# Kernel optimization log

Hardware: AMD Instinct MI355X
Metric: run time of the kernel (lower is better)

The kernel has to match this reference:

```python
import jax, jax.numpy as jnp
import numpy as np


def _square_distance(src, dst):
    # src: [B,N,C], dst: [B,M,C] -> [B,N,M] squared euclidean distances
    # ||s-d||^2 = -2 s.d + ||s||^2 + ||d||^2
    d = -2.0 * jnp.einsum('bnc,bmc->bnm', src, dst)
    d = d + jnp.sum(src * src, axis=-1)[:, :, None]
    d = d + jnp.sum(dst * dst, axis=-1)[:, None, :]
    return d


def setup_inputs() -> dict:
    key = jax.random.key(0)
    k1, k2 = jax.random.split(key)
    B, N, M, C = 8, 4096, 4096, 3
    f = jax.random.normal(k1, (B, N, C), dtype=jnp.float32)
    f_ = jax.random.normal(k2, (B, M, C), dtype=jnp.float32)
    return {"f": f, "f_": f_}


def reference(f, f_):
    dis = _square_distance(f, f_)          # [B,N,M]
    f2f_ = jnp.min(dis, axis=2)            # [B,N] nearest in f_ for each f point
    f_2f = jnp.min(dis, axis=1)            # [B,M] nearest in f for each f_ point
    d = jnp.mean(f2f_, axis=1) + jnp.mean(f_2f, axis=1)  # [B]
    return jnp.mean(d)
```

## Files before the change

### kernel.cpp

```cpp
#include <hip/hip_runtime.h>


typedef __attribute__((ext_vector_type(8))) short bf16x8;
typedef __attribute__((ext_vector_type(4))) float f32x4;

constexpr int B = 8;
constexpr int N = 4096;
constexpr int M = 4096;

constexpr int ROWS_PER_BLOCK = 128;
constexpr int COLS_PER_BLOCK = 2048;
constexpr int SEG = 512;
constexpr int SEGS = COLS_PER_BLOCK / SEG;
constexpr int TILES = SEG / 16;

static __device__ __forceinline__ unsigned short f2bf(float v) {
    unsigned u = __float_as_uint(v);
    return (unsigned short)((u + 0x7FFFu + ((u >> 16) & 1u)) >> 16);
}
static __device__ __forceinline__ float bf2f(unsigned short b) {
    return __uint_as_float(((unsigned)b) << 16);
}
static __device__ __forceinline__ void split3(float v, unsigned short& a,
                                              unsigned short& b, unsigned short& c) {
    a = f2bf(v); float r = v - bf2f(a);
    b = f2bf(r); r -= bf2f(b);
    c = f2bf(r);
}

__global__ __launch_bounds__(256, 4) void chamfer_dir_mfma(
    const float* __restrict__ f,
    const float* __restrict__ f_,
    unsigned int* __restrict__ minA,
    unsigned int* __restrict__ minB)
{
    __shared__ bf16x8 Bt[TILES * 64];

    const int tid  = threadIdx.x;
    const int lane = tid & 63;
    const int w    = tid >> 6;
    const int r    = lane & 15;
    const int kg   = lane >> 4;

    const int dir = blockIdx.z;
    const int b   = blockIdx.y;
    const int rc  = blockIdx.x >> 1;
    const int ch  = blockIdx.x & 1;

    const float* qsrc = dir ? f_ : f;
    const float* tsrc = dir ? f  : f_;
    unsigned int* omin = dir ? minB : minA;

    const int rowbase = rc * ROWS_PER_BLOCK + w * 32;
    bf16x8 afrag[2];
    #pragma unroll
    for (int rt = 0; rt < 2; ++rt) {
        const float* qp = qsrc + ((size_t)b * N + rowbase + rt * 16 + r) * 3;
        const float x = qp[0], y = qp[1], z = qp[2];
        unsigned short px0,px1,px2, py0,py1,py2, pz0,pz1,pz2, n0,n1,n2;
        split3(-2.f * x, px0, px1, px2);
        split3(-2.f * y, py0, py1, py2);
        split3(-2.f * z, pz0, pz1, pz2);
        split3(x*x + y*y + z*z, n0, n1, n2);
        const short ONE = 0x3F80;
        bf16x8 a;
        if (kg == 0)
            a = (bf16x8){(short)px0,(short)px0,(short)px1,(short)px1,(short)px0,(short)px2,(short)py0,(short)py0};
        else if (kg == 1)
            a = (bf16x8){(short)py1,(short)py1,(short)py0,(short)py2,(short)pz0,(short)pz0,(short)pz1,(short)pz1};
        else if (kg == 2)
            a = (bf16x8){(short)pz0,(short)pz2,(short)n0,(short)n1,(short)n2,ONE,ONE,ONE};
        else
            a = (bf16x8){0,0,0,0,0,0,0,0};
        afrag[rt] = a;
    }

    float rm[2][4];
    #pragma unroll
    for (int j = 0; j < 4; ++j) { rm[0][j] = 3.402823466e+38f; rm[1][j] = 3.402823466e+38f; }

    const float* tb = tsrc + ((size_t)b * M + (size_t)ch * COLS_PER_BLOCK) * 3;
    const f32x4 zero = {0.f, 0.f, 0.f, 0.f};

    for (int s = 0; s < SEGS; ++s) {
        __syncthreads();
        #pragma unroll
        for (int i = 0; i < 2; ++i) {
            const int t = i * 256 + tid;
            const float* tp = tb + (size_t)(s * SEG + t) * 3;
            const float x = tp[0], y = tp[1], z = tp[2];
            unsigned short x0,x1,x2, y0,y1,y2, z0,z1,z2, m0,m1,m2;
            split3(x, x0, x1, x2);
            split3(y, y0, y1, y2);
            split3(z, z0, z1, z2);
            split3(x*x + y*y + z*z, m0, m1, m2);
            const short ONE = 0x3F80;
            const int tile = t >> 4, rr = t & 15;
            bf16x8* base = &Bt[tile * 64 + rr];
            base[ 0] = (bf16x8){(short)x0,(short)x1,(short)x0,(short)x1,(short)x2,(short)x0,(short)y0,(short)y1};
            base[16] = (bf16x8){(short)y0,(short)y1,(short)y2,(short)y0,(short)z0,(short)z1,(short)z0,(short)z1};
            base[32] = (bf16x8){(short)z2,(short)z0,ONE,ONE,ONE,(short)m0,(short)m1,(short)m2};
            base[48] = (bf16x8){0,0,0,0,0,0,0,0};
        }
        __syncthreads();

        bf16x8 bb = Bt[lane];
        f32x4 pc0 = __builtin_amdgcn_mfma_f32_16x16x32_bf16(afrag[0], bb, zero, 0, 0, 0);
        f32x4 pc1 = __builtin_amdgcn_mfma_f32_16x16x32_bf16(afrag[1], bb, zero, 0, 0, 0);
        #pragma unroll 4
        for (int ct = 1; ct < TILES; ++ct) {
            bb = Bt[ct * 64 + lane];
            f32x4 c0 = __builtin_amdgcn_mfma_f32_16x16x32_bf16(afrag[0], bb, zero, 0, 0, 0);
            f32x4 c1 = __builtin_amdgcn_mfma_f32_16x16x32_bf16(afrag[1], bb, zero, 0, 0, 0);
            #pragma unroll
            for (int j = 0; j < 4; ++j) {
                rm[0][j] = fminf(rm[0][j], pc0[j]);
                rm[1][j] = fminf(rm[1][j], pc1[j]);
            }
            pc0 = c0; pc1 = c1;
        }
        #pragma unroll
        for (int j = 0; j < 4; ++j) {
            rm[0][j] = fminf(rm[0][j], pc0[j]);
            rm[1][j] = fminf(rm[1][j], pc1[j]);
        }
    }

    #pragma unroll
    for (int rt = 0; rt < 2; ++rt) {
        #pragma unroll
        for (int j = 0; j < 4; ++j) {
            float v = rm[rt][j];
            v = fminf(v, __shfl_xor(v, 1));
            v = fminf(v, __shfl_xor(v, 2));
            v = fminf(v, __shfl_xor(v, 4));
            v = fminf(v, __shfl_xor(v, 8));
            if (r == 0) {
                const int row = rowbase + rt * 16 + kg * 4 + j;
                atomicMin(&omin[b * N + row], __float_as_uint(v));
            }
        }
    }
}

__global__ __launch_bounds__(256) void reduce_out_kernel(
    const uint4* __restrict__ mins,
    float* __restrict__ out)
{
    __shared__ float wsum[4];
    const int tid = threadIdx.x;
    const uint4 v = mins[blockIdx.x * 256 + tid];
    float s = (__uint_as_float(v.x) + __uint_as_float(v.y))
            + (__uint_as_float(v.z) + __uint_as_float(v.w));

    #pragma unroll
    for (int off = 32; off > 0; off >>= 1) s += __shfl_down(s, off, 64);
    if ((tid & 63) == 0) wsum[tid >> 6] = s;
    __syncthreads();
    if (tid == 0) {
        const float r = (wsum[0] + wsum[1]) + (wsum[2] + wsum[3]);
        atomicAdd(out, r * (1.0f / 32768.0f));
    }
}

extern "C" void kernel_launch(void* const* d_in, const int* in_sizes, int n_in,
                              void* d_out, int out_size, void* d_ws, size_t ws_size,
                              hipStream_t stream) {
    (void)in_sizes; (void)n_in; (void)out_size; (void)ws_size;
    const float* f  = (const float*)d_in[0];
    const float* f_ = (const float*)d_in[1];
    float* out = (float*)d_out;

    unsigned int* minA = (unsigned int*)d_ws;
    unsigned int* minB = minA + (size_t)B * N;

    dim3 grid(64, 8, 2);
    chamfer_dir_mfma<<<grid, 256, 0, stream>>>(f, f_, minA, minB);

    reduce_out_kernel<<<64, 256, 0, stream>>>((const uint4*)minA, out);
}
```

Baseline: 73.51 us.

## Widen per-wave row tiles, drop zero LDS slab, double-buffer B fragment loads

Each wave now computes four 16-row query tiles instead of two, so every B fragment read from LDS feeds four MFMAs and the grid halves to 32 row-chunks per batch. The always-zero fourth 16-lane slab is no longer stored in shared memory; lanes with kg==3 keep a register zero instead. The inner loop prefetches the next two tiles' fragments while issuing eight MFMAs, then folds both results into the running minima. This trades higher register use (launch bounds drop to 2 waves) and half as many blocks for less LDS traffic and better MFMA issue density.

```diff
diff --git a/kernel.cpp b/kernel.cpp
--- a/kernel.cpp
+++ b/kernel.cpp
@@ -8,7 +8,8 @@
 constexpr int N = 4096;
 constexpr int M = 4096;
 
-constexpr int ROWS_PER_BLOCK = 128;
+constexpr int RT = 4;
+constexpr int ROWS_PER_BLOCK = 4 * RT * 16;
 constexpr int COLS_PER_BLOCK = 2048;
 constexpr int SEG = 512;
 constexpr int SEGS = COLS_PER_BLOCK / SEG;
@@ -28,13 +29,13 @@
     c = f2bf(r);
 }
 
-__global__ __launch_bounds__(256, 4) void chamfer_dir_mfma(
+__global__ __launch_bounds__(256, 2) void chamfer_dir_mfma(
     const float* __restrict__ f,
     const float* __restrict__ f_,
     unsigned int* __restrict__ minA,
     unsigned int* __restrict__ minB)
 {
-    __shared__ bf16x8 Bt[TILES * 64];
+    __shared__ bf16x8 Bt3[TILES * 48];
 
     const int tid  = threadIdx.x;
     const int lane = tid & 63;
@@ -51,10 +52,10 @@
     const float* tsrc = dir ? f  : f_;
     unsigned int* omin = dir ? minB : minA;
 
-    const int rowbase = rc * ROWS_PER_BLOCK + w * 32;
-    bf16x8 afrag[2];
+    const int rowbase = rc * ROWS_PER_BLOCK + w * (RT * 16);
+    bf16x8 afrag[RT];
     #pragma unroll
-    for (int rt = 0; rt < 2; ++rt) {
+    for (int rt = 0; rt < RT; ++rt) {
         const float* qp = qsrc + ((size_t)b * N + rowbase + rt * 16 + r) * 3;
         const float x = qp[0], y = qp[1], z = qp[2];
         unsigned short px0,px1,px2, py0,py1,py2, pz0,pz1,pz2, n0,n1,n2;
@@ -75,12 +76,15 @@
         afrag[rt] = a;
     }
 
-    float rm[2][4];
+    float rm[RT][4];
     #pragma unroll
-    for (int j = 0; j < 4; ++j) { rm[0][j] = 3.402823466e+38f; rm[1][j] = 3.402823466e+38f; }
+    for (int rt = 0; rt < RT; ++rt)
+        #pragma unroll
+        for (int j = 0; j < 4; ++j) rm[rt][j] = 3.402823466e+38f;
 
     const float* tb = tsrc + ((size_t)b * M + (size_t)ch * COLS_PER_BLOCK) * 3;
     const f32x4 zero = {0.f, 0.f, 0.f, 0.f};
+    const bf16x8 z8 = {0, 0, 0, 0, 0, 0, 0, 0};
 
     for (int s = 0; s < SEGS; ++s) {
         __syncthreads();
@@ -96,38 +100,40 @@
             split3(x*x + y*y + z*z, m0, m1, m2);
             const short ONE = 0x3F80;
             const int tile = t >> 4, rr = t & 15;
-            bf16x8* base = &Bt[tile * 64 + rr];
+            bf16x8* base = &Bt3[tile * 48 + rr];
             base[ 0] = (bf16x8){(short)x0,(short)x1,(short)x0,(short)x1,(short)x2,(short)x0,(short)y0,(short)y1};
             base[16] = (bf16x8){(short)y0,(short)y1,(short)y2,(short)y0,(short)z0,(short)z1,(short)z0,(short)z1};
             base[32] = (bf16x8){(short)z2,(short)z0,ONE,ONE,ONE,(short)m0,(short)m1,(short)m2};
-            base[48] = (bf16x8){0,0,0,0,0,0,0,0};
         }
         __syncthreads();
 
-        bf16x8 bb = Bt[lane];
-        f32x4 pc0 = __builtin_amdgcn_mfma_f32_16x16x32_bf16(afrag[0], bb, zero, 0, 0, 0);
-        f32x4 pc1 = __builtin_amdgcn_mfma_f32_16x16x32_bf16(afrag[1], bb, zero, 0, 0, 0);
-        #pragma unroll 4
-        for (int ct = 1; ct < TILES; ++ct) {
-            bb = Bt[ct * 64 + lane];
-            f32x4 c0 = __builtin_amdgcn_mfma_f32_16x16x32_bf16(afrag[0], bb, zero, 0, 0, 0);
-            f32x4 c1 = __builtin_amdgcn_mfma_f32_16x16x32_bf16(afrag[1], bb, zero, 0, 0, 0);
+        bf16x8 b0 = z8, b1 = z8, n0 = z8, n1 = z8;
+        if (kg < 3) { b0 = Bt3[lane]; b1 = Bt3[48 + lane]; }
+        #pragma unroll 2
+        for (int it = 0; it < TILES / 2; ++it) {
+            const int nt = (2 * it + 2) & (TILES - 1);
+            if (kg < 3) {
+                n0 = Bt3[nt * 48 + lane];
+                n1 = Bt3[(nt + 1) * 48 + lane];
+            }
+            f32x4 cA[RT], cB[RT];
             #pragma unroll
-            for (int j = 0; j < 4; ++j) {
-                rm[0][j] = fminf(rm[0][j], pc0[j]);
-                rm[1][j] = fminf(rm[1][j], pc1[j]);
-            }
-            pc0 = c0; pc1 = c1;
-        }
-        #pragma unroll
-        for (int j = 0; j < 4; ++j) {
-            rm[0][j] = fminf(rm[0][j], pc0[j]);
-            rm[1][j] = fminf(rm[1][j], pc1[j]);
+            for (int rt = 0; rt < RT; ++rt)
+                cA[rt] = __builtin_amdgcn_mfma_f32_16x16x32_bf16(afrag[rt], b0, zero, 0, 0, 0);
+            #pragma unroll
+            for (int rt = 0; rt < RT; ++rt)
+                cB[rt] = __builtin_amdgcn_mfma_f32_16x16x32_bf16(afrag[rt], b1, zero, 0, 0, 0);
+            #pragma unroll
+            for (int rt = 0; rt < RT; ++rt)
+                #pragma unroll
+                for (int j = 0; j < 4; ++j)
+                    rm[rt][j] = fminf(fminf(rm[rt][j], cA[rt][j]), cB[rt][j]);
+            b0 = n0; b1 = n1;
         }
     }
 
     #pragma unroll
-    for (int rt = 0; rt < 2; ++rt) {
+    for (int rt = 0; rt < RT; ++rt) {
         #pragma unroll
         for (int j = 0; j < 4; ++j) {
             float v = rm[rt][j];
@@ -174,7 +180,7 @@
     unsigned int* minA = (unsigned int*)d_ws;
     unsigned int* minB = minA + (size_t)B * N;
 
-    dim3 grid(64, 8, 2);
+    dim3 grid(32, 8, 2);
     chamfer_dir_mfma<<<grid, 256, 0, stream>>>(f, f_, minA, minB);
 
     reduce_out_kernel<<<64, 256, 0, stream>>>((const uint4*)minA, out);
```

New measurement: 77.17 us. +5.0%, slower.

## Fuse min and mean reduction into one kernel by giving each block all columns

Applied to the files above, without the earlier changes.

Each block now scans the full target set instead of half of it, so per-row minima are final inside the block. They are summed in-block and added straight to the output with one atomic per block. This removes the global atomicMin workspace and the separate reduction kernel launch. In exchange the grid is halved and each block runs a longer serial segment loop, with launch bounds relaxed to two blocks per CU.

```diff
diff --git a/kernel.cpp b/kernel.cpp
--- a/kernel.cpp
+++ b/kernel.cpp
@@ -9,9 +9,8 @@
 constexpr int M = 4096;
 
 constexpr int ROWS_PER_BLOCK = 128;
-constexpr int COLS_PER_BLOCK = 2048;
 constexpr int SEG = 512;
-constexpr int SEGS = COLS_PER_BLOCK / SEG;
+constexpr int SEGS = M / SEG;
 constexpr int TILES = SEG / 16;
 
 static __device__ __forceinline__ unsigned short f2bf(float v) {
@@ -28,13 +27,13 @@
     c = f2bf(r);
 }
 
-__global__ __launch_bounds__(256, 4) void chamfer_dir_mfma(
+__global__ __launch_bounds__(256, 2) void chamfer_rowsum(
     const float* __restrict__ f,
     const float* __restrict__ f_,
-    unsigned int* __restrict__ minA,
-    unsigned int* __restrict__ minB)
+    float* __restrict__ out)
 {
     __shared__ bf16x8 Bt[TILES * 64];
+    __shared__ float wsum[4];
 
     const int tid  = threadIdx.x;
     const int lane = tid & 63;
@@ -44,12 +43,10 @@
 
     const int dir = blockIdx.z;
     const int b   = blockIdx.y;
-    const int rc  = blockIdx.x >> 1;
-    const int ch  = blockIdx.x & 1;
+    const int rc  = blockIdx.x;
 
     const float* qsrc = dir ? f_ : f;
     const float* tsrc = dir ? f  : f_;
-    unsigned int* omin = dir ? minB : minA;
 
     const int rowbase = rc * ROWS_PER_BLOCK + w * 32;
     bf16x8 afrag[2];
@@ -79,7 +76,7 @@
     #pragma unroll
     for (int j = 0; j < 4; ++j) { rm[0][j] = 3.402823466e+38f; rm[1][j] = 3.402823466e+38f; }
 
-    const float* tb = tsrc + ((size_t)b * M + (size_t)ch * COLS_PER_BLOCK) * 3;
+    const float* tb = tsrc + (size_t)b * M * 3;
     const f32x4 zero = {0.f, 0.f, 0.f, 0.f};
 
     for (int s = 0; s < SEGS; ++s) {
@@ -126,6 +123,7 @@
         }
     }
 
+    float bsum = 0.f;
     #pragma unroll
     for (int rt = 0; rt < 2; ++rt) {
         #pragma unroll
@@ -135,47 +133,27 @@
             v = fminf(v, __shfl_xor(v, 2));
             v = fminf(v, __shfl_xor(v, 4));
             v = fminf(v, __shfl_xor(v, 8));
-            if (r == 0) {
-                const int row = rowbase + rt * 16 + kg * 4 + j;
-                atomicMin(&omin[b * N + row], __float_as_uint(v));
-            }
+            if (r == 0) bsum += v;
         }
     }
-}
-
-__global__ __launch_bounds__(256) void reduce_out_kernel(
-    const uint4* __restrict__ mins,
-    float* __restrict__ out)
-{
-    __shared__ float wsum[4];
-    const int tid = threadIdx.x;
-    const uint4 v = mins[blockIdx.x * 256 + tid];
-    float s = (__uint_as_float(v.x) + __uint_as_float(v.y))
-            + (__uint_as_float(v.z) + __uint_as_float(v.w));
-
     #pragma unroll
-    for (int off = 32; off > 0; off >>= 1) s += __shfl_down(s, off, 64);
-    if ((tid & 63) == 0) wsum[tid >> 6] = s;
+    for (int off = 32; off > 0; off >>= 1) bsum += __shfl_down(bsum, off, 64);
+    if (lane == 0) wsum[w] = bsum;
     __syncthreads();
     if (tid == 0) {
-        const float r = (wsum[0] + wsum[1]) + (wsum[2] + wsum[3]);
-        atomicAdd(out, r * (1.0f / 32768.0f));
+        const float rsum = (wsum[0] + wsum[1]) + (wsum[2] + wsum[3]);
+        atomicAdd(out, rsum * (1.0f / 32768.0f));
     }
 }
 
 extern "C" void kernel_launch(void* const* d_in, const int* in_sizes, int n_in,
                               void* d_out, int out_size, void* d_ws, size_t ws_size,
                               hipStream_t stream) {
-    (void)in_sizes; (void)n_in; (void)out_size; (void)ws_size;
+    (void)in_sizes; (void)n_in; (void)out_size; (void)ws_size; (void)d_ws;
     const float* f  = (const float*)d_in[0];
     const float* f_ = (const float*)d_in[1];
     float* out = (float*)d_out;
 
-    unsigned int* minA = (unsigned int*)d_ws;
-    unsigned int* minB = minA + (size_t)B * N;
-
-    dim3 grid(64, 8, 2);
-    chamfer_dir_mfma<<<grid, 256, 0, stream>>>(f, f_, minA, minB);
-
-    reduce_out_kernel<<<64, 256, 0, stream>>>((const uint4*)minA, out);
+    dim3 grid(32, 8, 2);
+    chamfer_rowsum<<<grid, 256, 0, stream>>>(f, f_, out);
 }
```

Result: slower. 78.80 us (+7.2%).
